# Kernel optimization log

Measured on AMD Instinct MI355X. Metric: run time of the kernel, lower is better.

## Reference

```python
import jax, jax.numpy as jnp
import numpy as np

DIM = 64
HEADS = 2
HD = DIM // HEADS          # 32
ALPHA = 4.0
KS = 5                     # dwc kernel size
MLP_H = 4 * DIM            # 256
LN_EPS = 1e-5


def layernorm(x, g, b):
    mu = jnp.mean(x, axis=-1, keepdims=True)
    var = jnp.mean(jnp.square(x - mu), axis=-1, keepdims=True)
    return (x - mu) * jax.lax.rsqrt(var + LN_EPS) * g + b


def safe_pow(x, p):
    # relu(x) ** p with well-defined value (and grad) at x <= 0
    xr = jnp.maximum(x, 0.0)
    safe = jnp.where(xr > 0, xr, 1.0)
    return jnp.where(xr > 0, safe ** p, 0.0)


def block_forward(x, H, W, ln1_g, ln1_b, w_qg, w_kv, pos_enc, scale_p, power_p,
                  dwc_w, dwc_b, w_proj, b_proj, ln2_g, ln2_b, w_fc1, b_fc1, w_fc2, b_fc2):
    B, N, C = x.shape
    h1 = layernorm(x, ln1_g, ln1_b)

    qg = h1 @ w_qg                         # [B,N,2C]
    q, gate = qg[..., :C], qg[..., C:]
    kv = h1 @ w_kv                         # [B,N,2C] (sr_ratio==1)
    k, v = kv[..., :C], kv[..., C:]
    k = k + pos_enc                        # [1,N,C]

    scale = jax.nn.softplus(scale_p)       # [1,1,C]
    power = 1.0 + ALPHA * jax.nn.sigmoid(power_p)  # [1,h,1,hd]
    q = q / scale
    k = k / scale

    # [B, h, N, hd]
    q = q.reshape(B, N, HEADS, HD).transpose(0, 2, 1, 3)
    k = k.reshape(B, N, HEADS, HD).transpose(0, 2, 1, 3)
    v = v.reshape(B, N, HEADS, HD).transpose(0, 2, 1, 3)

    q_pos = safe_pow(q, power)
    q_neg = safe_pow(-q, power)
    k_pos = safe_pow(k, power)
    k_neg = safe_pow(-k, power)

    q_sim = jnp.concatenate([q_pos, q_neg], axis=-1)   # [B,h,N,2hd]
    q_opp = jnp.concatenate([q_neg, q_pos], axis=-1)
    k_cat = jnp.concatenate([k_pos, k_neg], axis=-1)

    v1, v2 = v[..., :HD // 2], v[..., HD // 2:]

    n = N  # n_reduced == N for sr_ratio==1
    inv_sqrt_n = jnp.float32(n) ** -0.5
    k_mean = jnp.mean(k_cat, axis=-2)                  # [B,h,2hd]

    z_sim = 1.0 / (jnp.einsum('bhnd,bhd->bhn', q_sim, k_mean)[..., None] + 1e-6)
    kv_sim = jnp.einsum('bhnd,bhne->bhde', k_cat * inv_sqrt_n, v1 * inv_sqrt_n)
    x_sim = jnp.einsum('bhnd,bhde->bhne', q_sim, kv_sim) * z_sim

    z_opp = 1.0 / (jnp.einsum('bhnd,bhd->bhn', q_opp, k_mean)[..., None] + 1e-6)
    kv_opp = jnp.einsum('bhnd,bhne->bhde', k_cat * inv_sqrt_n, v2 * inv_sqrt_n)
    x_opp = jnp.einsum('bhnd,bhde->bhne', q_opp, kv_opp) * z_opp

    xa = jnp.concatenate([x_sim, x_opp], axis=-1)      # [B,h,N,hd]
    xa = xa.transpose(0, 2, 1, 3).reshape(B, N, C)

    # depthwise 5x5 conv over v in image layout
    v_img = v.reshape(B * HEADS, n, HD).transpose(0, 2, 1).reshape(B * HEADS, HD, H, W)
    v_dwc = jax.lax.conv_general_dilated(
        v_img, dwc_w, window_strides=(1, 1), padding='SAME',
        feature_group_count=HD, dimension_numbers=('NCHW', 'OIHW', 'NCHW'))
    v_dwc = v_dwc + dwc_b[None, :, None, None]
    v_dwc = v_dwc.reshape(B, C, H * W).transpose(0, 2, 1)  # [B,N,C]

    xa = (xa + v_dwc) * gate
    xa = xa @ w_proj + b_proj

    x = x + xa
    h2 = layernorm(x, ln2_g, ln2_b)
    m = jax.nn.gelu(h2 @ w_fc1 + b_fc1, approximate=False) @ w_fc2 + b_fc2
    return x + m


def setup_inputs() -> dict:
    key = jax.random.key(0)
    ks = jax.random.split(key, 12)
    B, H, W = 16, 128, 128
    N = H * W
    s = 0.02
    return {
        'x': jax.random.normal(ks[0], (B, N, DIM), jnp.float32),
        'H': H, 'W': W,
        'ln1_g': jnp.ones((DIM,), jnp.float32),
        'ln1_b': jnp.zeros((DIM,), jnp.float32),
        'w_qg': jax.random.normal(ks[1], (DIM, 2 * DIM), jnp.float32) * s,
        'w_kv': jax.random.normal(ks[2], (DIM, 2 * DIM), jnp.float32) * s,
        'pos_enc': jax.random.normal(ks[3], (1, N, DIM), jnp.float32) * s,
        'scale_p': jax.random.normal(ks[4], (1, 1, DIM), jnp.float32) * s,
        'power_p': jax.random.normal(ks[5], (1, HEADS, 1, HD), jnp.float32) * s,
        'dwc_w': jax.random.normal(ks[6], (HD, 1, KS, KS), jnp.float32) * s,
        'dwc_b': jnp.zeros((HD,), jnp.float32),
        'w_proj': jax.random.normal(ks[7], (DIM, DIM), jnp.float32) * s,
        'b_proj': jnp.zeros((DIM,), jnp.float32),
        'ln2_g': jnp.ones((DIM,), jnp.float32),
        'ln2_b': jnp.zeros((DIM,), jnp.float32),
        'w_fc1': jax.random.normal(ks[8], (DIM, MLP_H), jnp.float32) * s,
        'b_fc1': jnp.zeros((MLP_H,), jnp.float32),
        'w_fc2': jax.random.normal(ks[9], (MLP_H, DIM), jnp.float32) * s,
        'b_fc2': jnp.zeros((DIM,), jnp.float32),
    }


def reference(x, H, W, ln1_g, ln1_b, w_qg, w_kv, pos_enc, scale_p, power_p,
              dwc_w, dwc_b, w_proj, b_proj, ln2_g, ln2_b, w_fc1, b_fc1, w_fc2, b_fc2):
    return block_forward(x, H, W, ln1_g, ln1_b, w_qg, w_kv, pos_enc, scale_p, power_p,
                         dwc_w, dwc_b, w_proj, b_proj, ln2_g, ln2_b, w_fc1, b_fc1, w_fc2, b_fc2)
```

## Files before the change

kernel.cpp:

```cpp
#include <hip/hip_runtime.h>
#include <hip/hip_bf16.h>

#define NB 16
#define NT 16384
#define NTOK (NB * NT)

typedef __hip_bfloat16 bf16;
typedef __attribute__((ext_vector_type(8))) short short8;
typedef __attribute__((ext_vector_type(4))) float f32x4;

static __device__ __forceinline__ f32x4 MFMA(short8 a, short8 b, f32x4 c) {
    return __builtin_amdgcn_mfma_f32_16x16x32_bf16(a, b, c, 0, 0, 0);
}
static __device__ __forceinline__ short bfs(float f) {
    union { bf16 h; short s; } u; u.h = __float2bfloat16(f); return u.s;
}
static __device__ __forceinline__ float sbf(short s) {
    union { bf16 h; short s; } u; u.s = s; return __bfloat162float(u.h);
}
static __device__ __forceinline__ bf16 f2bf(float v) { return __float2bfloat16(v); }
static __device__ __forceinline__ float us2f(unsigned short u) {
    union { unsigned int i; float f; } x; x.i = ((unsigned int)u) << 16; return x.f;
}
static __device__ __forceinline__ unsigned char e8(float v) {
    union { _Float16 h; unsigned short u; } x; x.h = (_Float16)v;
    return (unsigned char)((x.u + 0x80) >> 8);
}
static __device__ __forceinline__ float d8(unsigned char e) {
    union { _Float16 h; unsigned short u; } x; x.u = (unsigned short)(e << 8);
    return (float)x.h;
}

static __device__ __forceinline__ float safe_pow(float x, float p) {
    return (x > 0.f) ? __builtin_amdgcn_exp2f(p * __builtin_amdgcn_logf(x)) : 0.f;
}
static __device__ __forceinline__ float sigm(float y) {
    return __builtin_amdgcn_rcpf(1.f + __builtin_amdgcn_exp2f(-1.44269504f * y));
}

static __device__ __forceinline__ int swb(int row, int tok) {
    return row * 64 + ((tok * 2) ^ (((row >> 1) & 3) << 4));
}

__global__ __launch_bounds__(256)
void k0_prep(const float* __restrict__ w_qg, const float* __restrict__ w_kv,
             const float* __restrict__ w_fc1, const float* __restrict__ w_fc2,
             short* __restrict__ wqk_f, short* __restrict__ wf1_f, short* __restrict__ wf2_f)
{
    int idx = blockIdx.x * 256 + threadIdx.x;
    if (idx < 16384) {
        int k = idx >> 8, col = idx & 255;
        float wv = (col < 128) ? w_qg[k * 128 + col] : w_kv[k * 128 + col - 128];
        int ct = col >> 4, ks = k >> 5, lane = (col & 15) + 16 * ((k & 31) >> 3), j = k & 7;
        wqk_f[((ct * 2 + ks) * 64 + lane) * 8 + j] = bfs(wv);
    } else if (idx < 32768) {
        int i2 = idx - 16384, k = i2 >> 8, col = i2 & 255;
        int ct = col >> 4, ks = k >> 5, lane = (col & 15) + 16 * ((k & 31) >> 3), j = k & 7;
        wf1_f[((ct * 2 + ks) * 64 + lane) * 8 + j] = bfs(w_fc1[k * 256 + col]);
    } else if (idx < 49152) {
        int i2 = idx - 32768, k = i2 >> 6, col = i2 & 63;
        int ct2 = col >> 4, ks = k >> 5, lane = (col & 15) + 16 * ((k & 31) >> 3), j = k & 7;
        wf2_f[((ct2 * 8 + ks) * 64 + lane) * 8 + j] = bfs(w_fc2[k * 64 + col]);
    }
}

__global__ __launch_bounds__(256)
void k1_proj(const float* __restrict__ x,
             const float* __restrict__ ln1_g, const float* __restrict__ ln1_b,
             const short* __restrict__ wqk_f,
             const float* __restrict__ pos_enc,
             const float* __restrict__ scale_p, const float* __restrict__ power_p,
             unsigned char* __restrict__ qb8, unsigned char* __restrict__ gbuf8,
             unsigned char* __restrict__ vbuf8,
             float* __restrict__ km_g, float* __restrict__ kv_g)
{
    __shared__ __align__(16) unsigned char lds[49152];
    __shared__ __align__(16) short wqk_s[16384];
    const int tid = threadIdx.x;
    const int b = blockIdx.y, chunk = blockIdx.x;
    const int w = tid >> 6, l = tid & 63, l15 = l & 15, g = l >> 4;
    unsigned char* kft = lds + w * 12288;
    unsigned char* vt  = kft + 8192;

    #pragma unroll
    for (int i = 0; i < 8; ++i)
        ((uint4*)wqk_s)[tid * 8 + i] = ((const uint4*)wqk_f)[tid * 8 + i];

    float g1v[16], b1v[16];
    #pragma unroll
    for (int j = 0; j < 8; j++) {
        g1v[j]     = ln1_g[g * 8 + j];      b1v[j]     = ln1_b[g * 8 + j];
        g1v[8 + j] = ln1_g[32 + g * 8 + j]; b1v[8 + j] = ln1_b[32 + g * 8 + j];
    }
    float isc[4], pwk[4];
    #pragma unroll
    for (int ct = 0; ct < 4; ct++) {
        int ch = l15 + 16 * ct;
        float s = scale_p[ch];
        float sp = 0.69314718f * __builtin_amdgcn_logf(1.f + __builtin_amdgcn_exp2f(1.44269504f * s));
        isc[ct] = __builtin_amdgcn_rcpf(sp);
        pwk[ct] = 1.f + 4.f * sigm(power_p[ch]);
    }

    f32x4 acc[2][2][4];
    #pragma unroll
    for (int s = 0; s < 2; s++)
        #pragma unroll
        for (int h = 0; h < 2; h++)
            #pragma unroll
            for (int mt = 0; mt < 4; mt++) { f32x4 z = {0.f,0.f,0.f,0.f}; acc[s][h][mt] = z; }
    float kmp[4] = {0.f,0.f,0.f,0.f}, kmn[4] = {0.f,0.f,0.f,0.f};

    __syncthreads();

    for (int it = 0; it < 8; ++it) {
        const int tok0 = chunk * 512 + (it * 4 + w) * 16;
        const size_t rowb = (size_t)b * NT + tok0;
        const float* xrow = x + (rowb + l15) * 64;
        float4 t0 = *(const float4*)(xrow + g * 8);
        float4 t1 = *(const float4*)(xrow + g * 8 + 4);
        float4 t2 = *(const float4*)(xrow + 32 + g * 8);
        float4 t3 = *(const float4*)(xrow + 32 + g * 8 + 4);
        float xa8[8] = {t0.x,t0.y,t0.z,t0.w,t1.x,t1.y,t1.z,t1.w};
        float xb8[8] = {t2.x,t2.y,t2.z,t2.w,t3.x,t3.y,t3.z,t3.w};
        float s1 = 0.f, s2 = 0.f;
        #pragma unroll
        for (int j = 0; j < 8; j++) {
            s1 += xa8[j] + xb8[j];
            s2 += xa8[j] * xa8[j] + xb8[j] * xb8[j];
        }
        s1 += __shfl_xor(s1, 16, 64); s1 += __shfl_xor(s1, 32, 64);
        s2 += __shfl_xor(s2, 16, 64); s2 += __shfl_xor(s2, 32, 64);
        float mu = s1 * 0.015625f;
        float var = s2 * 0.015625f - mu * mu;
        float rs = rsqrtf(var + 1e-5f);
        short8 A0, A1;
        #pragma unroll
        for (int j = 0; j < 8; j++) {
            A0[j] = bfs((xa8[j] - mu) * rs * g1v[j] + b1v[j]);
            A1[j] = bfs((xb8[j] - mu) * rs * g1v[8 + j] + b1v[8 + j]);
        }
        const int tokp = (it & 1) * 16;
        #pragma unroll
        for (int ct = 0; ct < 16; ct++) {
            short8 f0 = *(const short8*)(wqk_s + (ct * 2 + 0) * 512 + l * 8);
            short8 f1 = *(const short8*)(wqk_s + (ct * 2 + 1) * 512 + l * 8);
            f32x4 c = {0.f,0.f,0.f,0.f};
            c = MFMA(A0, f0, c);
            c = MFMA(A1, f1, c);
            if (ct < 4) {
                #pragma unroll
                for (int r = 0; r < 4; r++)
                    qb8[(rowb + g * 4 + r) * 64 + l15 + 16 * ct] = e8(c[r] * isc[ct]);
            } else if (ct < 8) {
                #pragma unroll
                for (int r = 0; r < 4; r++)
                    gbuf8[(rowb + g * 4 + r) * 64 + l15 + 16 * (ct - 4)] = e8(c[r]);
            } else if (ct < 12) {
                const int ctk = ct - 8, kchan = l15 + 16 * ctk;
                const int hh = kchan >> 5, d = kchan & 31;
                #pragma unroll
                for (int r = 0; r < 4; r++) {
                    int n = tok0 + g * 4 + r;
                    float kvl = (c[r] + pos_enc[(size_t)n * 64 + kchan]) * isc[ctk];
                    float kp = safe_pow(kvl, pwk[ctk]);
                    float kn = safe_pow(-kvl, pwk[ctk]);
                    kmp[ctk] += kp; kmn[ctk] += kn;
                    int tk = tokp + g * 4 + r;
                    *(short*)(kft + swb(hh * 64 + d, tk))      = bfs(kp);
                    *(short*)(kft + swb(hh * 64 + 32 + d, tk)) = bfs(kn);
                }
            } else {
                const int ctv = ct - 12, vchan = l15 + 16 * ctv;
                const int hh = vchan >> 5, vc = vchan & 31;
                #pragma unroll
                for (int r = 0; r < 4; r++) {
                    int tk = tokp + g * 4 + r;
                    vbuf8[(rowb + g * 4 + r) * 64 + vchan] = e8(c[r]);
                    *(short*)(vt + swb(hh * 32 + vc, tk)) = bfs(c[r]);
                }
            }
        }
        if (it & 1) {
            #pragma unroll
            for (int h = 0; h < 2; h++) {
                int rv0 = h * 32 + l15, rv1 = h * 32 + 16 + l15;
                short8 Bv0 = *(const short8*)(vt + rv0 * 64 + ((g * 16) ^ (((rv0 >> 1) & 3) << 4)));
                short8 Bv1 = *(const short8*)(vt + rv1 * 64 + ((g * 16) ^ (((rv1 >> 1) & 3) << 4)));
                #pragma unroll
                for (int mt = 0; mt < 4; mt++) {
                    int rk = h * 64 + mt * 16 + l15;
                    short8 Ak = *(const short8*)(kft + rk * 64 + ((g * 16) ^ (((rk >> 1) & 3) << 4)));
                    acc[0][h][mt] = MFMA(Ak, Bv0, acc[0][h][mt]);
                    acc[1][h][mt] = MFMA(Ak, Bv1, acc[1][h][mt]);
                }
            }
        }
    }
    const float invN = 1.f / 16384.f;
    float* kvb = kv_g + (size_t)b * 4096;
    #pragma unroll
    for (int s = 0; s < 2; s++)
        #pragma unroll
        for (int h = 0; h < 2; h++)
            #pragma unroll
            for (int mt = 0; mt < 4; mt++)
                #pragma unroll
                for (int r = 0; r < 4; r++)
                    atomicAdd(&kvb[((s * 2 + h) * 64 + mt * 16 + g * 4 + r) * 16 + l15],
                              acc[s][h][mt][r] * invN);
    #pragma unroll
    for (int ct = 0; ct < 4; ct++) {
        kmp[ct] += __shfl_xor(kmp[ct], 16, 64); kmp[ct] += __shfl_xor(kmp[ct], 32, 64);
        kmn[ct] += __shfl_xor(kmn[ct], 16, 64); kmn[ct] += __shfl_xor(kmn[ct], 32, 64);
    }
    if (g == 0) {
        #pragma unroll
        for (int ct = 0; ct < 4; ct++) {
            int kchan = l15 + 16 * ct, hh = kchan >> 5, d = kchan & 31;
            atomicAdd(&km_g[b * 128 + hh * 64 + d],      kmp[ct] * invN);
            atomicAdd(&km_g[b * 128 + hh * 64 + 32 + d], kmn[ct] * invN);
        }
    }
}

__global__ __launch_bounds__(256)
void k2_dwc(const unsigned char* __restrict__ vbuf8,
            const float* __restrict__ dwc_w, const float* __restrict__ dwc_b,
            unsigned char* __restrict__ vdb8)
{
    __shared__ __align__(16) unsigned short tile[12][36][64];
    const int tid = threadIdx.x;
    const int b = blockIdx.y;
    const int ty = blockIdx.x >> 2, tx = blockIdx.x & 3;
    const int y0 = ty * 8, x0 = tx * 32;

    #pragma unroll
    for (int i = 0; i < 14; ++i) {
        int cid = i * 256 + tid;
        if (cid < 3456) {
            int yy = cid / 288;
            int rem = cid - yy * 288;
            int xx = rem >> 3;
            int c8 = rem & 7;
            int Y = y0 - 2 + yy, X = x0 - 2 + xx;
            uint2 val = make_uint2(0u, 0u);
            if ((unsigned)Y < 128u && (unsigned)X < 128u)
                val = *(const uint2*)(vbuf8 + (((size_t)b * NT + Y * 128 + X) * 64 + c8 * 8));
            unsigned short ob[8];
            #pragma unroll
            for (int k = 0; k < 4; k++) {
                ob[k]     = (unsigned short)bfs(d8((unsigned char)(val.x >> (8 * k))));
                ob[4 + k] = (unsigned short)bfs(d8((unsigned char)(val.y >> (8 * k))));
            }
            uint4 o;
            o.x = (unsigned)ob[0] | ((unsigned)ob[1] << 16);
            o.y = (unsigned)ob[2] | ((unsigned)ob[3] << 16);
            o.z = (unsigned)ob[4] | ((unsigned)ob[5] << 16);
            o.w = (unsigned)ob[6] | ((unsigned)ob[7] << 16);
            *(uint4*)(&tile[yy][xx][c8 * 8]) = o;
        }
    }
    __syncthreads();

    const int w = tid >> 6, c = tid & 63, d = c & 31;
    float wt[25];
    #pragma unroll
    for (int k = 0; k < 25; k++) wt[k] = dwc_w[d * 25 + k];
    const float bias = dwc_b[d];

    #pragma unroll
    for (int yl2 = 0; yl2 < 2; ++yl2) {
        const int yl = w * 2 + yl2;
        float cw[5][5];
        #pragma unroll
        for (int xx = 0; xx < 4; ++xx)
            #pragma unroll
            for (int ky = 0; ky < 5; ++ky)
                cw[ky][xx] = us2f(tile[yl + ky][xx][c]);
        #pragma unroll
        for (int xl = 0; xl < 32; ++xl) {
            const int jn = (xl + 4) % 5;
            #pragma unroll
            for (int ky = 0; ky < 5; ++ky)
                cw[ky][jn] = us2f(tile[yl + ky][xl + 4][c]);
            float acc = bias;
            #pragma unroll
            for (int ky = 0; ky < 5; ++ky)
                #pragma unroll
                for (int kx = 0; kx < 5; ++kx)
                    acc += wt[ky * 5 + kx] * cw[ky][(xl + kx) % 5];
            const int Y = y0 + yl, X = x0 + xl;
            vdb8[((size_t)b * NT + Y * 128 + X) * 64 + c] = e8(acc);
        }
    }
}

__global__ __launch_bounds__(1024, 4)
void k3_main(const float* __restrict__ x,
             const unsigned char* __restrict__ qb8, const unsigned char* __restrict__ gbuf8,
             const unsigned char* __restrict__ vdb8,
             const float* __restrict__ km_g, const float* __restrict__ kv_g,
             const float* __restrict__ power_p,
             const float* __restrict__ w_proj, const float* __restrict__ b_proj,
             const float* __restrict__ ln2_g, const float* __restrict__ ln2_b,
             const short* __restrict__ wf1_f, const short* __restrict__ wf2_f,
             const float* __restrict__ b_fc1, const float* __restrict__ b_fc2,
             float* __restrict__ out)
{
    __shared__ __align__(16) short wkv_s[8][512];
    __shared__ __align__(16) short wp_s[8][512];
    __shared__ __align__(16) short wf1_s[16384];
    __shared__ __align__(16) short wf2_s[16384];
    __shared__ __align__(16) unsigned char tbuf[16][2048];

    const int tid = threadIdx.x, b = blockIdx.y, chunk = blockIdx.x;
    const int w = tid >> 6, l = tid & 63, l15 = l & 15, g = l >> 4;
    unsigned char* tb = tbuf[w];

    if (tid < 512) {
        int frag = tid >> 6, lane = tid & 63;
        int s2h = frag >> 1, ks = frag & 1;
        short8 v;
        #pragma unroll
        for (int j = 0; j < 8; ++j) {
            int idx = s2h * 1024 + (ks * 32 + (lane >> 4) * 8 + j) * 16 + (lane & 15);
            v[j] = bfs(kv_g[(size_t)b * 4096 + idx]);
        }
        *(short8*)&wkv_s[frag][lane * 8] = v;
    } else {
        int t2 = tid - 512;
        int frag = t2 >> 6, lane = t2 & 63;
        int ct = frag >> 1, ks = frag & 1;
        short8 v;
        #pragma unroll
        for (int j = 0; j < 8; ++j) {
            int idx = (ks * 32 + (lane >> 4) * 8 + j) * 64 + ct * 16 + (lane & 15);
            v[j] = bfs(w_proj[idx]);
        }
        *(short8*)&wp_s[frag][lane * 8] = v;
    }
    #pragma unroll
    for (int i = 0; i < 2; ++i) {
        ((uint4*)wf1_s)[tid * 2 + i] = ((const uint4*)wf1_f)[tid * 2 + i];
        ((uint4*)wf2_s)[tid * 2 + i] = ((const uint4*)wf2_f)[tid * 2 + i];
    }

    short8 Kden[2][2];
    #pragma unroll
    for (int h = 0; h < 2; ++h)
        #pragma unroll
        for (int f = 0; f < 2; ++f)
            #pragma unroll
            for (int j = 0; j < 8; ++j) {
                int d = g * 8 + j;
                float v = 0.f;
                if (l15 == 0)      v = km_g[b * 128 + h * 64 + (f ? 32 + d : d)];
                else if (l15 == 1) v = km_g[b * 128 + h * 64 + (f ? d : 32 + d)];
                Kden[h][f][j] = bfs(v);
            }

    float pw3[2][8];
    #pragma unroll
    for (int h = 0; h < 2; h++)
        #pragma unroll
        for (int j = 0; j < 8; j++)
            pw3[h][j] = 1.f + 4.f * sigm(power_p[h * 32 + g * 8 + j]);
    float bpj[4], g2[4], b2[4], bfc2v[4];
    #pragma unroll
    for (int ct = 0; ct < 4; ct++) {
        int ch = l15 + 16 * ct;
        bpj[ct] = b_proj[ch]; g2[ct] = ln2_g[ch]; b2[ct] = ln2_b[ch]; bfc2v[ct] = b_fc2[ch];
    }
    float bf1v[16];
    #pragma unroll
    for (int ct = 0; ct < 16; ct++) bf1v[ct] = b_fc1[ct * 16 + l15];

    __syncthreads();

    for (int it = 0; it < 2; ++it) {
        const int tok0 = chunk * 512 + (it * 16 + w) * 16;
        const size_t rowb = (size_t)b * NT + tok0;
        const size_t goff = (rowb + l15) * 64;

        float qf[2][8], vdf[2][8], ggf[2][8];
        #pragma unroll
        for (int ks = 0; ks < 2; ks++) {
            uint2 qv = *(const uint2*)(qb8   + goff + ks * 32 + g * 8);
            uint2 gv = *(const uint2*)(gbuf8 + goff + ks * 32 + g * 8);
            uint2 vv = *(const uint2*)(vdb8  + goff + ks * 32 + g * 8);
            #pragma unroll
            for (int k = 0; k < 4; k++) {
                qf[ks][k]      = d8((unsigned char)(qv.x >> (8 * k)));
                qf[ks][4 + k]  = d8((unsigned char)(qv.y >> (8 * k)));
                ggf[ks][k]     = d8((unsigned char)(gv.x >> (8 * k)));
                ggf[ks][4 + k] = d8((unsigned char)(gv.y >> (8 * k)));
                vdf[ks][k]     = d8((unsigned char)(vv.x >> (8 * k)));
                vdf[ks][4 + k] = d8((unsigned char)(vv.y >> (8 * k)));
            }
        }
        float xv[4][4];
        #pragma unroll
        for (int ct = 0; ct < 4; ct++)
            #pragma unroll
            for (int r = 0; r < 4; r++)
                xv[ct][r] = x[(rowb + g * 4 + r) * 64 + l15 + 16 * ct];

        short8 Fqp[2], Fqn[2];
        f32x4 dn[2];
        #pragma unroll
        for (int h = 0; h < 2; h++) {
            #pragma unroll
            for (int j = 0; j < 8; j++) {
                float q = qf[h][j];
                Fqp[h][j] = bfs(safe_pow(q, pw3[h][j]));
                Fqn[h][j] = bfs(safe_pow(-q, pw3[h][j]));
            }
            f32x4 z4 = {0.f, 0.f, 0.f, 0.f};
            z4 = MFMA(Fqp[h], Kden[h][0], z4);
            dn[h] = MFMA(Fqn[h], Kden[h][1], z4);
        }

        f32x4 at[4];
        #pragma unroll
        for (int hs = 0; hs < 4; hs++) { f32x4 z4 = {0.f,0.f,0.f,0.f}; at[hs] = z4; }
        #pragma unroll
        for (int h = 0; h < 2; h++) {
            short8 b00 = *(const short8*)&wkv_s[(0 * 2 + h) * 2 + 0][l * 8];
            short8 b01 = *(const short8*)&wkv_s[(0 * 2 + h) * 2 + 1][l * 8];
            short8 b10 = *(const short8*)&wkv_s[(1 * 2 + h) * 2 + 0][l * 8];
            short8 b11 = *(const short8*)&wkv_s[(1 * 2 + h) * 2 + 1][l * 8];
            at[h*2+0] = MFMA(Fqp[h], b00, at[h*2+0]);
            at[h*2+0] = MFMA(Fqn[h], b01, at[h*2+0]);
            at[h*2+1] = MFMA(Fqn[h], b10, at[h*2+1]);
            at[h*2+1] = MFMA(Fqp[h], b11, at[h*2+1]);
        }

        #pragma unroll
        for (int hs = 0; hs < 4; hs++) {
            int h = hs >> 1, s = hs & 1;
            int cb = h * 32 + s * 16;
            #pragma unroll
            for (int r = 0; r < 4; r++) {
                float dv = __shfl(dn[h][r], g * 16 + s, 64);
                float zz = __builtin_amdgcn_rcpf(dv + 1e-6f);
                int tok = g * 4 + r;
                *(short*)(tb + tok * 128 + (((cb + l15) * 2) ^ ((tok & 7) << 4))) = bfs(at[hs][r] * zz);
            }
        }
        short8 Ap[2];
        #pragma unroll
        for (int ks = 0; ks < 2; ks++) {
            short8 t8 = *(short8*)(tb + l15 * 128 + ((ks * 64 + g * 16) ^ ((l15 & 7) << 4)));
            #pragma unroll
            for (int j = 0; j < 8; j++)
                Ap[ks][j] = bfs((sbf(t8[j]) + vdf[ks][j]) * ggf[ks][j]);
        }

        f32x4 pc[4];
        #pragma unroll
        for (int ct = 0; ct < 4; ct++) {
            short8 w0 = *(const short8*)&wp_s[ct * 2 + 0][l * 8];
            short8 w1 = *(const short8*)&wp_s[ct * 2 + 1][l * 8];
            f32x4 z4 = {0.f,0.f,0.f,0.f};
            z4 = MFMA(Ap[0], w0, z4);
            pc[ct] = MFMA(Ap[1], w1, z4);
        }

        float xm[4][4];
        #pragma unroll
        for (int ct = 0; ct < 4; ct++)
            #pragma unroll
            for (int r = 0; r < 4; r++)
                xm[ct][r] = xv[ct][r] + pc[ct][r] + bpj[ct];
        #pragma unroll
        for (int r = 0; r < 4; r++) {
            float s1 = xm[0][r] + xm[1][r] + xm[2][r] + xm[3][r];
            float s2 = xm[0][r]*xm[0][r] + xm[1][r]*xm[1][r] + xm[2][r]*xm[2][r] + xm[3][r]*xm[3][r];
            #pragma unroll
            for (int m = 1; m < 16; m <<= 1) { s1 += __shfl_xor(s1, m, 64); s2 += __shfl_xor(s2, m, 64); }
            float mu = s1 * 0.015625f;
            float var = s2 * 0.015625f - mu * mu;
            float rs = rsqrtf(var + 1e-5f);
            int tok = g * 4 + r;
            #pragma unroll
            for (int ct = 0; ct < 4; ct++) {
                float h2 = (xm[ct][r] - mu) * rs * g2[ct] + b2[ct];
                *(short*)(tb + tok * 128 + (((ct * 16 + l15) * 2) ^ ((tok & 7) << 4))) = bfs(h2);
            }
        }
        short8 Ah[2];
        #pragma unroll
        for (int ks = 0; ks < 2; ks++)
            Ah[ks] = *(short8*)(tb + l15 * 128 + ((ks * 64 + g * 16) ^ ((l15 & 7) << 4)));

        f32x4 a2[4];
        #pragma unroll
        for (int ct = 0; ct < 4; ct++) { f32x4 z4 = {0.f,0.f,0.f,0.f}; a2[ct] = z4; }
        #pragma unroll
        for (int g4 = 0; g4 < 4; g4++) {
            f32x4 fc[4];
            #pragma unroll
            for (int ctl = 0; ctl < 4; ctl++) {
                int ct = g4 * 4 + ctl;
                short8 f0 = *(const short8*)(wf1_s + (ct * 2 + 0) * 512 + l * 8);
                short8 f1 = *(const short8*)(wf1_s + (ct * 2 + 1) * 512 + l * 8);
                f32x4 z4 = {0.f,0.f,0.f,0.f};
                z4 = MFMA(Ah[0], f0, z4);
                fc[ctl] = MFMA(Ah[1], f1, z4);
            }
            #pragma unroll
            for (int ctl = 0; ctl < 4; ctl++)
                #pragma unroll
                for (int r = 0; r < 4; r++) {
                    float mv = fc[ctl][r] + bf1v[g4 * 4 + ctl];
                    float gl = mv * __builtin_amdgcn_rcpf(1.f +
                        __builtin_amdgcn_exp2f(mv * (-2.30220825f - 0.10294385f * mv * mv)));
                    int tok = g * 4 + r;
                    *(short*)(tb + tok * 128 + (((ctl * 16 + l15) * 2) ^ ((tok & 7) << 4))) = bfs(gl);
                }
            #pragma unroll
            for (int ksl = 0; ksl < 2; ksl++) {
                short8 Ag = *(short8*)(tb + l15 * 128 + ((ksl * 64 + g * 16) ^ ((l15 & 7) << 4)));
                int ks = g4 * 2 + ksl;
                #pragma unroll
                for (int ct2 = 0; ct2 < 4; ct2++) {
                    short8 wv = *(const short8*)(wf2_s + (ct2 * 8 + ks) * 512 + l * 8);
                    a2[ct2] = MFMA(Ag, wv, a2[ct2]);
                }
            }
        }

        float* tb32 = (float*)tb;
        #pragma unroll
        for (int half = 0; half < 2; ++half) {
            #pragma unroll
            for (int ctl = 0; ctl < 2; ++ctl) {
                int ct = half * 2 + ctl;
                #pragma unroll
                for (int r = 0; r < 4; r++)
                    tb32[(g * 4 + r) * 32 + ctl * 16 + l15] = xm[ct][r] + a2[ct][r] + bfc2v[ct];
            }
            #pragma unroll
            for (int i = 0; i < 2; ++i) {
                f32x4 v = *(f32x4*)&tb32[i * 256 + l * 4];
                *(f32x4*)(out + (rowb + i * 8 + (l >> 3)) * 64 + half * 32 + (l & 7) * 4) = v;
            }
        }
    }
}

extern "C" void kernel_launch(void* const* d_in, const int* in_sizes, int n_in,
                              void* d_out, int out_size, void* d_ws, size_t ws_size,
                              hipStream_t stream)
{
    const float* x       = (const float*)d_in[0];
    const float* ln1_g   = (const float*)d_in[3];
    const float* ln1_b   = (const float*)d_in[4];
    const float* w_qg    = (const float*)d_in[5];
    const float* w_kv    = (const float*)d_in[6];
    const float* pos     = (const float*)d_in[7];
    const float* scale_p = (const float*)d_in[8];
    const float* power_p = (const float*)d_in[9];
    const float* dwc_w   = (const float*)d_in[10];
    const float* dwc_b   = (const float*)d_in[11];
    const float* w_proj  = (const float*)d_in[12];
    const float* b_proj  = (const float*)d_in[13];
    const float* ln2_g   = (const float*)d_in[14];
    const float* ln2_b   = (const float*)d_in[15];
    const float* w_fc1   = (const float*)d_in[16];
    const float* b_fc1   = (const float*)d_in[17];
    const float* w_fc2   = (const float*)d_in[18];
    const float* b_fc2   = (const float*)d_in[19];
    float* out = (float*)d_out;

    size_t ntc = (size_t)NTOK * 64;
    unsigned char* qb8   = (unsigned char*)d_ws;
    unsigned char* vbuf8 = qb8 + ntc;
    unsigned char* gbuf8 = vbuf8 + ntc;
    unsigned char* vdb8  = gbuf8 + ntc;
    float* km_g = (float*)(vdb8 + ntc);
    float* kv_g = km_g + (size_t)NB * 128;
    short* wqk_f = (short*)(kv_g + (size_t)NB * 4096);
    short* wf1_f = wqk_f + 16384;
    short* wf2_f = wf1_f + 16384;

    hipMemsetAsync(km_g, 0, ((size_t)NB * 128 + (size_t)NB * 4096) * sizeof(float), stream);

    k0_prep<<<dim3(192), 256, 0, stream>>>(w_qg, w_kv, w_fc1, w_fc2, wqk_f, wf1_f, wf2_f);
    k1_proj<<<dim3(32, NB), 256, 0, stream>>>(x, ln1_g, ln1_b, wqk_f, pos, scale_p, power_p,
                                              qb8, gbuf8, vbuf8, km_g, kv_g);
    k2_dwc<<<dim3(64, NB), 256, 0, stream>>>(vbuf8, dwc_w, dwc_b, vdb8);
    k3_main<<<dim3(32, NB), 1024, 0, stream>>>(x, qb8, gbuf8, vdb8, km_g, kv_g, power_p,
                                               w_proj, b_proj, ln2_g, ln2_b,
                                               wf1_f, wf2_f, b_fc1, b_fc2, out);
}
```

Measured before the change: 236.2 us.

## Prefetch next tile's inputs in k3_main and halve grid with more tokens per block

The main fused kernel now handles 1024 tokens per block over four iterations instead of 512 over two, and the grid is halved to match. Each iteration issues the global loads (q, gate, dwc'd v, residual x) for the next tile before computing the current one, so memory latency overlaps compute. Per-block setup such as the weight staging and Kden is also amortized over more tokens. The cost is higher register pressure from double-buffered inputs, and only 256 blocks of 1024 threads may underfill the GPU.

Result: no change. 234.0 us, median of 2 (-1.0%).

```diff
diff --git a/kernel.cpp b/kernel.cpp
--- a/kernel.cpp
+++ b/kernel.cpp
@@ -378,33 +378,49 @@
 
     __syncthreads();
 
-    for (int it = 0; it < 2; ++it) {
-        const int tok0 = chunk * 512 + (it * 16 + w) * 16;
+    auto LOADIT = [&](int itx, uint2* qv, uint2* gv, uint2* vv, float (*xvv)[4]) {
+        const int tok0 = chunk * 1024 + (itx * 16 + w) * 16;
         const size_t rowb = (size_t)b * NT + tok0;
         const size_t goff = (rowb + l15) * 64;
+        #pragma unroll
+        for (int ks = 0; ks < 2; ks++) {
+            qv[ks] = *(const uint2*)(qb8   + goff + ks * 32 + g * 8);
+            gv[ks] = *(const uint2*)(gbuf8 + goff + ks * 32 + g * 8);
+            vv[ks] = *(const uint2*)(vdb8  + goff + ks * 32 + g * 8);
+        }
+        #pragma unroll
+        for (int ct = 0; ct < 4; ct++)
+            #pragma unroll
+            for (int r = 0; r < 4; r++)
+                xvv[ct][r] = x[(rowb + g * 4 + r) * 64 + l15 + 16 * ct];
+    };
+
+    uint2 qv[2], gv[2], vv[2];
+    float xv[4][4];
+    LOADIT(0, qv, gv, vv, xv);
+
+    #pragma unroll
+    for (int it = 0; it < 4; ++it) {
+        uint2 qv2[2], gv2[2], vv2[2];
+        float xv2[4][4];
+        if (it < 3) LOADIT(it + 1, qv2, gv2, vv2, xv2);
+
+        const int tok0 = chunk * 1024 + (it * 16 + w) * 16;
+        const size_t rowb = (size_t)b * NT + tok0;
 
         float qf[2][8], vdf[2][8], ggf[2][8];
         #pragma unroll
         for (int ks = 0; ks < 2; ks++) {
-            uint2 qv = *(const uint2*)(qb8   + goff + ks * 32 + g * 8);
-            uint2 gv = *(const uint2*)(gbuf8 + goff + ks * 32 + g * 8);
-            uint2 vv = *(const uint2*)(vdb8  + goff + ks * 32 + g * 8);
             #pragma unroll
             for (int k = 0; k < 4; k++) {
-                qf[ks][k]      = d8((unsigned char)(qv.x >> (8 * k)));
-                qf[ks][4 + k]  = d8((unsigned char)(qv.y >> (8 * k)));
-                ggf[ks][k]     = d8((unsigned char)(gv.x >> (8 * k)));
-                ggf[ks][4 + k] = d8((unsigned char)(gv.y >> (8 * k)));
-                vdf[ks][k]     = d8((unsigned char)(vv.x >> (8 * k)));
-                vdf[ks][4 + k] = d8((unsigned char)(vv.y >> (8 * k)));
-            }
-        }
-        float xv[4][4];
-        #pragma unroll
-        for (int ct = 0; ct < 4; ct++)
-            #pragma unroll
-            for (int r = 0; r < 4; r++)
-                xv[ct][r] = x[(rowb + g * 4 + r) * 64 + l15 + 16 * ct];
+                qf[ks][k]      = d8((unsigned char)(qv[ks].x >> (8 * k)));
+                qf[ks][4 + k]  = d8((unsigned char)(qv[ks].y >> (8 * k)));
+                ggf[ks][k]     = d8((unsigned char)(gv[ks].x >> (8 * k)));
+                ggf[ks][4 + k] = d8((unsigned char)(gv[ks].y >> (8 * k)));
+                vdf[ks][k]     = d8((unsigned char)(vv[ks].x >> (8 * k)));
+                vdf[ks][4 + k] = d8((unsigned char)(vv[ks].y >> (8 * k)));
+            }
+        }
 
         short8 Fqp[2], Fqn[2];
         f32x4 dn[2];
@@ -547,6 +563,14 @@
                 *(f32x4*)(out + (rowb + i * 8 + (l >> 3)) * 64 + half * 32 + (l & 7) * 4) = v;
             }
         }
+
+        #pragma unroll
+        for (int ks = 0; ks < 2; ks++) { qv[ks] = qv2[ks]; gv[ks] = gv2[ks]; vv[ks] = vv2[ks]; }
+        #pragma unroll
+        for (int ct = 0; ct < 4; ct++)
+            #pragma unroll
+            for (int r = 0; r < 4; r++)
+                xv[ct][r] = xv2[ct][r];
     }
 }
 
@@ -591,7 +615,7 @@
     k1_proj<<<dim3(32, NB), 256, 0, stream>>>(x, ln1_g, ln1_b, wqk_f, pos, scale_p, power_p,
                                               qb8, gbuf8, vbuf8, km_g, kv_g);
     k2_dwc<<<dim3(64, NB), 256, 0, stream>>>(vbuf8, dwc_w, dwc_b, vdb8);
-    k3_main<<<dim3(32, NB), 1024, 0, stream>>>(x, qb8, gbuf8, vdb8, km_g, kv_g, power_p,
+    k3_main<<<dim3(16, NB), 1024, 0, stream>>>(x, qb8, gbuf8, vdb8, km_g, kv_g, power_p,
                                                w_proj, b_proj, ln2_g, ln2_b,
                                                wf1_f, wf2_f, b_fc1, b_fc2, out);
 }
```
